# Optimization experiments

Measured on AMD Instinct MI355X. Metric: run time of the kernel, lower is better.

The kernel has to match this reference:

```python
import jax, jax.numpy as jnp
import numpy as np

EMBED_DIM = 256
NUM_HEADS = 4
LN_EPS = 1e-5


def setup_inputs() -> dict:
    b, n, e = 2, 4096, EMBED_DIM
    key = jax.random.key(0)
    ks = jax.random.split(key, 12)
    x = jax.random.normal(ks[0], (b, n, e), dtype=jnp.float32)
    # rotary cache: cos/sin of random angles, shape [2, b, n, e, 1]
    ang = jax.random.uniform(ks[1], (b, n, e, 1), dtype=jnp.float32) * (2 * np.pi)
    encoding = jnp.stack([jnp.cos(ang), jnp.sin(ang)], axis=0)
    s_e = 1.0 / np.sqrt(e)
    s_2e = 1.0 / np.sqrt(2 * e)
    Wqkv_w = jax.random.normal(ks[2], (3 * e, e), dtype=jnp.float32) * s_e
    Wqkv_b = jax.random.normal(ks[3], (3 * e,), dtype=jnp.float32) * s_e
    out_w = jax.random.normal(ks[4], (e, e), dtype=jnp.float32) * s_e
    out_b = jax.random.normal(ks[5], (e,), dtype=jnp.float32) * s_e
    ffn1_w = jax.random.normal(ks[6], (2 * e, 2 * e), dtype=jnp.float32) * s_2e
    ffn1_b = jax.random.normal(ks[7], (2 * e,), dtype=jnp.float32) * s_2e
    ln_g = jnp.ones((2 * e,), dtype=jnp.float32)
    ln_b = jnp.zeros((2 * e,), dtype=jnp.float32)
    ffn2_w = jax.random.normal(ks[8], (e, 2 * e), dtype=jnp.float32) * s_2e
    ffn2_b = jax.random.normal(ks[9], (e,), dtype=jnp.float32) * s_2e
    return {"x": x, "encoding": encoding, "Wqkv_w": Wqkv_w, "Wqkv_b": Wqkv_b,
            "out_w": out_w, "out_b": out_b, "ffn1_w": ffn1_w, "ffn1_b": ffn1_b,
            "ln_g": ln_g, "ln_b": ln_b, "ffn2_w": ffn2_w, "ffn2_b": ffn2_b}


def _forward(x, encoding, Wqkv_w, Wqkv_b, out_w, out_b, ffn1_w, ffn1_b, ln_g, ln_b, ffn2_w, ffn2_b):
    b, n, e = x.shape
    h = NUM_HEADS
    hd = e // h
    qkv = x @ Wqkv_w.T + Wqkv_b                      # [b,n,3e]
    qkv = qkv.reshape(b, n, e, 3)
    qk, v = qkv[..., :2], qkv[..., 2]                # [b,n,e,2], [b,n,e]
    # rotate_half: interpret e as (h, hd//2, 2) pairs, rotate within pairs
    r = qk.reshape(b, n, h, hd // 2, 2, 2)
    r = jnp.stack([-r[..., 1, :], r[..., 0, :]], axis=4).reshape(b, n, e, 2)
    qk = qk * encoding[0] + r * encoding[1]          # cached rotary emb
    q = qk[..., 0].reshape(b, n, h, hd)
    k = qk[..., 1].reshape(b, n, h, hd)
    vh = v.reshape(b, n, h, hd)
    scale = 1.0 / np.sqrt(hd).astype(np.float32)
    scores = jnp.einsum('bqhd,bkhd->bhqk', q, k) * scale
    attn = jax.nn.softmax(scores, axis=-1)
    ctx = jnp.einsum('bhqk,bkhd->bqhd', attn, vh).reshape(b, n, e)
    message = ctx @ out_w.T + out_b
    y = jnp.concatenate([x, message], axis=2)        # [b,n,2e]
    y = y @ ffn1_w.T + ffn1_b
    mu = jnp.mean(y, axis=-1, keepdims=True)
    var = jnp.mean(jnp.square(y - mu), axis=-1, keepdims=True)
    y = (y - mu) * jax.lax.rsqrt(var + LN_EPS) * ln_g + ln_b
    y = jax.nn.gelu(y, approximate=False)            # torch nn.GELU default = exact
    y = y @ ffn2_w.T + ffn2_b
    return x + y


def reference(x, encoding, Wqkv_w, Wqkv_b, out_w, out_b, ffn1_w, ffn1_b, ln_g, ln_b, ffn2_w, ffn2_b):
    return _forward(x, encoding, Wqkv_w, Wqkv_b, out_w, out_b, ffn1_w, ffn1_b, ln_g, ln_b, ffn2_w, ffn2_b)
```

## Files before the change

### kernel.cpp

```cpp
#include <hip/hip_runtime.h>
#include <hip/hip_bf16.h>

using u16 = unsigned short;
using u16x8 = __attribute__((ext_vector_type(8))) unsigned short;
using s16x4 = __attribute__((ext_vector_type(4))) short;
using s16x8 = __attribute__((ext_vector_type(8))) short;
using f32x4 = __attribute__((ext_vector_type(4))) float;

__device__ __forceinline__ f32x4 mfma16(s16x8 a, s16x8 b, f32x4 c) {
    return __builtin_amdgcn_mfma_f32_16x16x32_bf16(a, b, c, 0, 0, 0);
}

__device__ __forceinline__ u16 f2bf(float f) {
    union { float f; unsigned u; } v; v.f = f;
    unsigned r = v.u + 0x7FFFu + ((v.u >> 16) & 1u);
    return (u16)(r >> 16);
}

__device__ __forceinline__ unsigned cvt_pk_bf16(float lo, float hi) {
    unsigned r;
    asm("v_cvt_pk_bf16_f32 %0, %1, %2" : "=v"(r) : "v"(lo), "v"(hi));
    return r;
}

__device__ __forceinline__ float fast_exp2(float x) {
    float r;
    asm("v_exp_f32 %0, %1" : "=v"(r) : "v"(x));
    return r;
}

__device__ __forceinline__ unsigned pk2(u16 a, u16 b) {
    return (unsigned)a | ((unsigned)b << 16);
}

__device__ __forceinline__ float bf2f(u16 u) {
    union { unsigned u; float f; } v; v.u = ((unsigned)u) << 16;
    return v.f;
}

__device__ __forceinline__ void gload_lds16(const u16* g, u16* l) {
    __builtin_amdgcn_global_load_lds(
        (const __attribute__((address_space(1))) void*)g,
        (__attribute__((address_space(3))) void*)l, 16, 0, 0);
}

__global__ __launch_bounds__(256) void conv_kernel(
    const float* __restrict__ s0, const float* __restrict__ s1,
    const float* __restrict__ s2, const float* __restrict__ s3,
    const float* __restrict__ s4,
    u16* __restrict__ d0, u16* __restrict__ d1, u16* __restrict__ d2,
    u16* __restrict__ d3, u16* __restrict__ d4)
{
    int i = blockIdx.x * 256 + threadIdx.x;
    const float* s; u16* d; int off;
    if (i < 524288)      { s = s0; d = d0; off = i; }
    else if (i < 573440) { s = s1; d = d1; off = i - 524288; }
    else if (i < 589824) { s = s2; d = d2; off = i - 573440; }
    else if (i < 655360) { s = s3; d = d3; off = i - 589824; }
    else                 { s = s4; d = d4; off = i - 655360; }
    float4 f = ((const float4*)s)[off];
    ushort4 u;
    u.x = f2bf(f.x); u.y = f2bf(f.y); u.z = f2bf(f.z); u.w = f2bf(f.w);
    ((ushort4*)d)[off] = u;
}

template<int OUTMODE, bool SPLIT, bool RESID, bool BIAS, int BM>
__global__ __launch_bounds__(256) void gemm_kernel(
    const u16* __restrict__ A0, const u16* __restrict__ A1,
    const u16* __restrict__ W0, const float* __restrict__ bias,
    const float* __restrict__ resid, float* __restrict__ outf,
    u16* __restrict__ outb,
    int M, int N, int K, int lda0, int lda1, int ldw0, int ldo)
{
    constexpr int MS = BM / 32;
    __shared__ u16 A_lds[3][BM][64];
    __shared__ u16 B_lds[3][64][64];
    const int tid = threadIdx.x;
    const int l = tid & 63, w = tid >> 6;
    const int lr = l & 15, lg = l >> 4;
    const int r7 = lr & 7;
    const int m0 = blockIdx.x * BM, n0 = blockIdx.y * 64;
    const int wm = (w >> 1) * (BM / 2), wn = (w & 1) * 32;

    const int lrow = l >> 3;
    const int swz = (l & 7) ^ lrow;
    const int arow = (BM / 4) * w + lrow;
    const int brow = 16 * w + lrow;

    #define STAGE_G(s, b)                                                     \
        do {                                                                  \
            int k0_ = 64 * (s);                                               \
            const u16* As_; int lda_; int ka_ = k0_;                          \
            if (SPLIT && k0_ >= 256) { As_ = A1; lda_ = lda1; ka_ = k0_ - 256; }\
            else { As_ = A0; lda_ = lda0; }                                   \
            _Pragma("unroll")                                                 \
            for (int i = 0; i < BM / 32; ++i)                                 \
                gload_lds16(As_ + (size_t)(m0 + arow + 8 * i) * lda_ + ka_ + swz * 8,\
                            &A_lds[b][(BM / 4) * w + 8 * i][0]);              \
            _Pragma("unroll")                                                 \
            for (int i = 0; i < 2; ++i)                                       \
                gload_lds16(W0 + (size_t)(n0 + brow + 8 * i) * ldw0 + k0_ + swz * 8,\
                            &B_lds[b][16 * w + 8 * i][0]);                    \
        } while (0)

    f32x4 acc[MS][2];
    #pragma unroll
    for (int i = 0; i < MS; ++i)
        #pragma unroll
        for (int j = 0; j < 2; ++j)
            acc[i][j] = (f32x4){0.f, 0.f, 0.f, 0.f};

    const int NS = K >> 6;
    int cur = 0, nxt = 1;
    STAGE_G(0, 0);

    for (int s = 0; s < NS; ++s) {
        if (s + 1 < NS) {
            STAGE_G(s + 1, nxt);
            if constexpr (BM == 128)
                asm volatile("s_waitcnt vmcnt(6)" ::: "memory");
            else
                asm volatile("s_waitcnt vmcnt(4)" ::: "memory");
        } else {
            asm volatile("s_waitcnt vmcnt(0)" ::: "memory");
        }
        __builtin_amdgcn_sched_barrier(0);
        __builtin_amdgcn_s_barrier();
        __builtin_amdgcn_sched_barrier(0);

        #pragma unroll
        for (int ks = 0; ks < 2; ++ks) {
            s16x8 af[MS], bfr[2];
            #pragma unroll
            for (int ms = 0; ms < MS; ++ms)
                af[ms] = *(const s16x8*)&A_lds[cur][wm + ms * 16 + lr]
                                              [((ks * 4 + lg) ^ r7) * 8];
            #pragma unroll
            for (int ns = 0; ns < 2; ++ns)
                bfr[ns] = *(const s16x8*)&B_lds[cur][wn + ns * 16 + lr]
                                               [((ks * 4 + lg) ^ r7) * 8];
            #pragma unroll
            for (int ms = 0; ms < MS; ++ms)
                #pragma unroll
                for (int ns = 0; ns < 2; ++ns)
                    acc[ms][ns] = mfma16(af[ms], bfr[ns], acc[ms][ns]);
        }
        cur = nxt;
        nxt = (nxt == 2) ? 0 : nxt + 1;
    }
    #undef STAGE_G

    #pragma unroll
    for (int ms = 0; ms < MS; ++ms) {
        #pragma unroll
        for (int ns = 0; ns < 2; ++ns) {
            int cg = n0 + wn + ns * 16 + lr;
            float bv = BIAS ? bias[cg] : 0.f;
            #pragma unroll
            for (int r = 0; r < 4; ++r) {
                int rg = m0 + wm + ms * 16 + lg * 4 + r;
                float val = acc[ms][ns][r] + bv;
                if (RESID) val += resid[(size_t)rg * N + cg];
                if (OUTMODE == 0) outf[(size_t)rg * ldo + cg] = val;
                else              outb[(size_t)rg * ldo + cg] = f2bf(val);
            }
        }
    }
}

__global__ __launch_bounds__(256) void rope_tv_kernel(
    const u16* __restrict__ qkv, const float* __restrict__ enc,
    u16* __restrict__ Qo, u16* __restrict__ Ko, u16* __restrict__ Vt)
{
    __shared__ u16 vt_lds[64][72];
    const int tid = threadIdx.x;
    const int bh = blockIdx.y, n0 = blockIdx.x * 64;
    const int b = bh >> 2, h = bh & 3;
    const float qs = 0.18033688011112042f;

    #pragma unroll
    for (int it = 0; it < 8; ++it) {
        int task = it * 256 + tid;
        int r = task >> 5, t = task & 31;
        size_t grow = (size_t)(b * 4096 + n0 + r);
        const u16* base = qkv + grow * 768 + 3 * (h * 64) + 6 * t;
        ushort2 a01 = *(const ushort2*)(base);
        ushort2 a23 = *(const ushort2*)(base + 2);
        ushort2 a45 = *(const ushort2*)(base + 4);
        float q0 = bf2f(a01.x), k0 = bf2f(a01.y);
        float q1 = bf2f(a23.y), k1 = bf2f(a45.x);
        const float* cb = enc + grow * 256 + h * 64 + 2 * t;
        float2 cosv = *(const float2*)cb;
        float2 sinv = *(const float2*)(cb + 2097152);
        float qr0 = (q0 * cosv.x - q1 * sinv.x) * qs;
        float qr1 = (q1 * cosv.y + q0 * sinv.y) * qs;
        float kr0 = k0 * cosv.x - k1 * sinv.x;
        float kr1 = k1 * cosv.y + k0 * sinv.y;
        size_t o = ((size_t)bh * 4096 + n0 + r) * 64 + 2 * t;
        *(unsigned*)(Qo + o) = cvt_pk_bf16(qr0, qr1);
        *(unsigned*)(Ko + o) = cvt_pk_bf16(kr0, kr1);
        vt_lds[r][2 * t]     = a23.x;
        vt_lds[r][2 * t + 1] = a45.y;
    }
    __syncthreads();
    #pragma unroll
    for (int i = 0; i < 2; ++i) {
        int c = tid + 256 * i;
        int d = c >> 3, ng = c & 7;
        int kb = ng >> 2, lg4 = ng & 3;
        int base = 32 * kb + 4 * lg4;
        unsigned w0 = pk2(vt_lds[base +  0][d], vt_lds[base +  1][d]);
        unsigned w1 = pk2(vt_lds[base +  2][d], vt_lds[base +  3][d]);
        unsigned w2 = pk2(vt_lds[base + 16][d], vt_lds[base + 17][d]);
        unsigned w3 = pk2(vt_lds[base + 18][d], vt_lds[base + 19][d]);
        uint4 o4 = make_uint4(w0, w1, w2, w3);
        *(uint4*)(Vt + ((size_t)bh * 64 + d) * 4096 + n0 + ng * 8) = o4;
    }
}

__global__ __launch_bounds__(256) void attn_kernel(
    const u16* __restrict__ Qp, const u16* __restrict__ Kp,
    const u16* __restrict__ Vtp, u16* __restrict__ Opart,
    float* __restrict__ Ssum)
{
    __shared__ u16 K_lds[2][64][64];
    __shared__ u16 V_lds[2][64][64];
    const int tid = threadIdx.x;
    const int l = tid & 63, w = tid >> 6;
    const int lr = l & 15, lg = l >> 4;
    const int r7 = lr & 7;
    const int bh = blockIdx.y, z = blockIdx.z;
    const int n0 = blockIdx.x * 128 + w * 32;

    const u16* Qb = Qp + ((size_t)bh * 4096 + n0) * 64;
    s16x8 qf[2][2];
    #pragma unroll
    for (int qt = 0; qt < 2; ++qt)
        #pragma unroll
        for (int dh = 0; dh < 2; ++dh)
            qf[qt][dh] = *(const s16x8*)(Qb + (qt * 16 + lr) * 64 + dh * 32 + lg * 8);

    const u16* Kb = Kp + (size_t)bh * 4096 * 64 + (size_t)z * 1024 * 64;
    const u16* Vb = Vtp + (size_t)bh * 64 * 4096 + z * 1024;

    const int xs0 = (lg ^ r7) * 8;
    const int xs1 = ((4 + lg) ^ r7) * 8;

    const int swz = (l & 7) ^ ((l >> 3) & 7);
    const int row0 = 16 * w + (l >> 3);
    const size_t koff0 = (size_t)row0 * 64 + swz * 8;
    const size_t koff1 = (size_t)(row0 + 8) * 64 + swz * 8;
    const size_t voff0 = (size_t)row0 * 4096 + swz * 8;
    const size_t voff1 = (size_t)(row0 + 8) * 4096 + swz * 8;

    #define STAGE(kt, b)                                                      \
        do {                                                                  \
            const u16* ks_ = Kb + (size_t)(kt) * 4096;                        \
            const u16* vs_ = Vb + (size_t)(kt) * 64;                          \
            gload_lds16(ks_ + koff0, &K_lds[b][16 * w][0]);                   \
            gload_lds16(ks_ + koff1, &K_lds[b][16 * w + 8][0]);               \
            gload_lds16(vs_ + voff0, &V_lds[b][16 * w][0]);                   \
            gload_lds16(vs_ + voff1, &V_lds[b][16 * w + 8][0]);               \
        } while (0)

    f32x4 O[2][4];
    #pragma unroll
    for (int qt = 0; qt < 2; ++qt)
        #pragma unroll
        for (int dv = 0; dv < 4; ++dv)
            O[qt][dv] = (f32x4){0.f, 0.f, 0.f, 0.f};
    f32x4 ssum[2];
    ssum[0] = (f32x4){0.f, 0.f, 0.f, 0.f};
    ssum[1] = (f32x4){0.f, 0.f, 0.f, 0.f};
    s16x8 ones;
    #pragma unroll
    for (int j = 0; j < 8; ++j) ones[j] = (short)0x3F80;

    STAGE(0, 0);
    __syncthreads();

    #define PHASE(kt, CB, DO_STAGE)                                           \
        do {                                                                  \
            if (DO_STAGE) STAGE((kt) + 1, (CB) ^ 1);                          \
            f32x4 S[2][4];                                                    \
            __builtin_amdgcn_s_setprio(1);                                    \
            _Pragma("unroll")                                                 \
            for (int v4 = 0; v4 < 4; ++v4) {                                  \
                const int krow = v4 * 16 + lr;                                \
                s16x8 kf0 = *(const s16x8*)&K_lds[CB][krow][xs0];             \
                s16x8 kf1 = *(const s16x8*)&K_lds[CB][krow][xs1];             \
                _Pragma("unroll")                                             \
                for (int qt = 0; qt < 2; ++qt) {                              \
                    f32x4 zz = (f32x4){-24.f, -24.f, -24.f, -24.f};           \
                    zz = mfma16(kf0, qf[qt][0], zz);                          \
                    zz = mfma16(kf1, qf[qt][1], zz);                          \
                    S[qt][v4] = zz;                                           \
                }                                                             \
            }                                                                 \
            __builtin_amdgcn_s_setprio(0);                                    \
            s16x8 pa[2][2];                                                   \
            _Pragma("unroll")                                                 \
            for (int qt = 0; qt < 2; ++qt) {                                  \
                float p[4][4];                                                \
                _Pragma("unroll")                                             \
                for (int v4 = 0; v4 < 4; ++v4)                                \
                    _Pragma("unroll")                                         \
                    for (int r = 0; r < 4; ++r)                               \
                        p[v4][r] = fast_exp2(S[qt][v4][r]);                   \
                _Pragma("unroll")                                             \
                for (int kb = 0; kb < 2; ++kb) {                              \
                    union { unsigned u[4]; s16x8 v; } pu;                     \
                    pu.u[0] = cvt_pk_bf16(p[2*kb][0],   p[2*kb][1]);          \
                    pu.u[1] = cvt_pk_bf16(p[2*kb][2],   p[2*kb][3]);          \
                    pu.u[2] = cvt_pk_bf16(p[2*kb+1][0], p[2*kb+1][1]);        \
                    pu.u[3] = cvt_pk_bf16(p[2*kb+1][2], p[2*kb+1][3]);        \
                    pa[qt][kb] = pu.v;                                        \
                }                                                             \
            }                                                                 \
            __builtin_amdgcn_s_setprio(1);                                    \
            _Pragma("unroll")                                                 \
            for (int dv = 0; dv < 4; ++dv) {                                  \
                const int vrow = 16 * dv + lr;                                \
                s16x8 vf0 = *(const s16x8*)&V_lds[CB][vrow][xs0];             \
                s16x8 vf1 = *(const s16x8*)&V_lds[CB][vrow][xs1];             \
                _Pragma("unroll")                                             \
                for (int qt = 0; qt < 2; ++qt) {                              \
                    O[qt][dv] = mfma16(pa[qt][0], vf0, O[qt][dv]);            \
                    O[qt][dv] = mfma16(pa[qt][1], vf1, O[qt][dv]);            \
                }                                                             \
            }                                                                 \
            _Pragma("unroll")                                                 \
            for (int qt = 0; qt < 2; ++qt) {                                  \
                ssum[qt] = mfma16(pa[qt][0], ones, ssum[qt]);                 \
                ssum[qt] = mfma16(pa[qt][1], ones, ssum[qt]);                 \
            }                                                                 \
            __builtin_amdgcn_s_setprio(0);                                    \
            __syncthreads();                                                  \
        } while (0)

    #pragma unroll 1
    for (int kt = 0; kt < 16; kt += 2) {
        PHASE(kt, 0, true);
        PHASE(kt + 1, 1, kt < 14);
    }
    #undef PHASE
    #undef STAGE

    u16* Ob = Opart + ((size_t)(z * 8 + bh) * 4096 + n0) * 64;
    #pragma unroll
    for (int qt = 0; qt < 2; ++qt)
        #pragma unroll
        for (int dv = 0; dv < 4; ++dv)
            #pragma unroll
            for (int r = 0; r < 4; ++r)
                Ob[(size_t)(qt * 16 + 4 * lg + r) * 64 + 16 * dv + lr] =
                    f2bf(O[qt][dv][r]);
    if (lr == 0) {
        #pragma unroll
        for (int qt = 0; qt < 2; ++qt) {
            float4 sv = make_float4(ssum[qt][0], ssum[qt][1],
                                    ssum[qt][2], ssum[qt][3]);
            *(float4*)&Ssum[(size_t)(z * 8 + bh) * 4096 + n0 + qt * 16 + 4 * lg] = sv;
        }
    }
}

__global__ __launch_bounds__(256) void combine_kernel(
    const u16* __restrict__ Opart, const float* __restrict__ Ssum,
    u16* __restrict__ ctx)
{
    int idx = blockIdx.x * 256 + threadIdx.x;
    int rr = idx >> 3;
    int dc = (idx & 7) * 8;
    float s = Ssum[rr] + Ssum[32768 + rr] + Ssum[65536 + rr] + Ssum[98304 + rr];
    float inv = 1.f / s;
    float acc[8];
    #pragma unroll
    for (int j = 0; j < 8; ++j) acc[j] = 0.f;
    #pragma unroll
    for (int z = 0; z < 4; ++z) {
        u16x8 ov = *(const u16x8*)(Opart + ((size_t)z * 32768 + rr) * 64 + dc);
        #pragma unroll
        for (int j = 0; j < 8; ++j) acc[j] += bf2f(ov[j]);
    }
    #pragma unroll
    for (int j = 0; j < 8; ++j) acc[j] *= inv;
    int bh = rr >> 12, n = rr & 4095;
    int b = bh >> 2, h = bh & 3;
    uint4 o4 = make_uint4(cvt_pk_bf16(acc[0], acc[1]), cvt_pk_bf16(acc[2], acc[3]),
                          cvt_pk_bf16(acc[4], acc[5]), cvt_pk_bf16(acc[6], acc[7]));
    *(uint4*)(ctx + ((size_t)(b * 4096 + n)) * 256 + h * 64 + dc) = o4;
}

__global__ __launch_bounds__(256) void ln_gelu_kernel(
    const u16* __restrict__ y, const float* __restrict__ g,
    const float* __restrict__ bta, u16* __restrict__ o)
{
    int row = blockIdx.x * 4 + (threadIdx.x >> 6);
    int l = threadIdx.x & 63;
    const u16* yr = y + (size_t)row * 512 + l * 8;
    u16x8 uv = *(const u16x8*)yr;
    float v[8];
    #pragma unroll
    for (int j = 0; j < 8; ++j) v[j] = bf2f(uv[j]);
    float s = 0.f;
    #pragma unroll
    for (int j = 0; j < 8; ++j) s += v[j];
    #pragma unroll
    for (int off = 32; off; off >>= 1) s += __shfl_xor(s, off, 64);
    float mu = s * (1.f / 512.f);
    float q = 0.f;
    #pragma unroll
    for (int j = 0; j < 8; ++j) { float t = v[j] - mu; q += t * t; }
    #pragma unroll
    for (int off = 32; off; off >>= 1) q += __shfl_xor(q, off, 64);
    float rs = rsqrtf(q * (1.f / 512.f) + 1e-5f);
    u16 u[8];
    #pragma unroll
    for (int j = 0; j < 8; ++j) {
        float t = (v[j] - mu) * rs * g[l * 8 + j] + bta[l * 8 + j];
        t = t * 0.5f * (1.f + erff(t * 0.70710678118654752f));
        u[j] = f2bf(t);
    }
    uint4 o4 = make_uint4(pk2(u[0], u[1]), pk2(u[2], u[3]),
                          pk2(u[4], u[5]), pk2(u[6], u[7]));
    *(uint4*)(o + (size_t)row * 512 + l * 8) = o4;
}

extern "C" void kernel_launch(void* const* d_in, const int* in_sizes, int n_in,
                              void* d_out, int out_size, void* d_ws, size_t ws_size,
                              hipStream_t stream) {
    (void)in_sizes; (void)n_in; (void)out_size; (void)ws_size;
    const float* x    = (const float*)d_in[0];
    const float* enc  = (const float*)d_in[1];
    const float* wqkv = (const float*)d_in[2];
    const float* bqkv = (const float*)d_in[3];
    const float* wout = (const float*)d_in[4];
    const float* bout = (const float*)d_in[5];
    const float* w1   = (const float*)d_in[6];
    const float* b1   = (const float*)d_in[7];
    const float* lng  = (const float*)d_in[8];
    const float* lnb  = (const float*)d_in[9];
    const float* w2   = (const float*)d_in[10];
    const float* b2   = (const float*)d_in[11];
    float* out = (float*)d_out;
    char* ws = (char*)d_ws;

    u16*   xb    = (u16*)(ws + 0);
    u16*   wqkvb = (u16*)(ws + 4194304);
    u16*   woutb = (u16*)(ws + 4587520);
    u16*   w1b   = (u16*)(ws + 4718592);
    u16*   w2b   = (u16*)(ws + 5242880);
    u16*   qkvb  = (u16*)(ws + 5505024);
    u16*   OpartB= (u16*)(ws + 5505024);
    u16*   y1bf  = (u16*)(ws + 5505024);
    float* Ssum  = (float*)(ws + 22282240);
    u16*   q     = (u16*)(ws + 30670848);
    u16*   k     = (u16*)(ws + 34865152);
    u16*   vt    = (u16*)(ws + 43253760);
    u16*   ybf   = q;
    u16*   ctx   = (u16*)(ws + 47448064);
    u16*   msg   = (u16*)(ws + 51642368);

    conv_kernel<<<2688, 256, 0, stream>>>(x, wqkv, wout, w1, w2,
                                          xb, wqkvb, woutb, w1b, w2b);
    gemm_kernel<1, false, false, true, 128><<<dim3(64, 12), 256, 0, stream>>>(
        xb, nullptr, wqkvb, bqkv, nullptr, nullptr, qkvb,
        8192, 768, 256, 256, 0, 256, 768);
    rope_tv_kernel<<<dim3(64, 8), 256, 0, stream>>>(qkvb, enc, q, k, vt);
    attn_kernel<<<dim3(32, 8, 4), 256, 0, stream>>>(q, k, vt, OpartB, Ssum);
    combine_kernel<<<1024, 256, 0, stream>>>(OpartB, Ssum, ctx);
    gemm_kernel<1, false, false, true, 64><<<dim3(128, 4), 256, 0, stream>>>(
        ctx, nullptr, woutb, bout, nullptr, nullptr, msg,
        8192, 256, 256, 256, 0, 256, 256);
    gemm_kernel<1, true, false, true, 128><<<dim3(64, 8), 256, 0, stream>>>(
        xb, msg, w1b, b1, nullptr, nullptr, y1bf,
        8192, 512, 512, 256, 256, 512, 512);
    ln_gelu_kernel<<<2048, 256, 0, stream>>>(y1bf, lng, lnb, ybf);
    gemm_kernel<0, false, true, true, 64><<<dim3(128, 4), 256, 0, stream>>>(
        ybf, nullptr, w2b, b2, x, out, nullptr,
        8192, 256, 512, 512, 0, 512, 256);
}
```

Baseline: 116.5 us.

## Double per-wave query rows in attention and split key block into two passes

```diff
diff --git a/kernel.cpp b/kernel.cpp
--- a/kernel.cpp
+++ b/kernel.cpp
@@ -230,12 +230,12 @@
     const int lr = l & 15, lg = l >> 4;
     const int r7 = lr & 7;
     const int bh = blockIdx.y, z = blockIdx.z;
-    const int n0 = blockIdx.x * 128 + w * 32;
+    const int n0 = blockIdx.x * 256 + w * 64;
 
     const u16* Qb = Qp + ((size_t)bh * 4096 + n0) * 64;
-    s16x8 qf[2][2];
-    #pragma unroll
-    for (int qt = 0; qt < 2; ++qt)
+    s16x8 qf[4][2];
+    #pragma unroll
+    for (int qt = 0; qt < 4; ++qt)
         #pragma unroll
         for (int dh = 0; dh < 2; ++dh)
             qf[qt][dh] = *(const s16x8*)(Qb + (qt * 16 + lr) * 64 + dh * 32 + lg * 8);
@@ -263,78 +263,80 @@
             gload_lds16(vs_ + voff1, &V_lds[b][16 * w + 8][0]);               \
         } while (0)
 
-    f32x4 O[2][4];
-    #pragma unroll
-    for (int qt = 0; qt < 2; ++qt)
+    f32x4 O[4][4];
+    #pragma unroll
+    for (int qt = 0; qt < 4; ++qt)
         #pragma unroll
         for (int dv = 0; dv < 4; ++dv)
             O[qt][dv] = (f32x4){0.f, 0.f, 0.f, 0.f};
-    f32x4 ssum[2];
-    ssum[0] = (f32x4){0.f, 0.f, 0.f, 0.f};
-    ssum[1] = (f32x4){0.f, 0.f, 0.f, 0.f};
+    f32x4 ssum[4];
+    #pragma unroll
+    for (int qt = 0; qt < 4; ++qt) ssum[qt] = (f32x4){0.f, 0.f, 0.f, 0.f};
     s16x8 ones;
     #pragma unroll
     for (int j = 0; j < 8; ++j) ones[j] = (short)0x3F80;
 
     STAGE(0, 0);
     __syncthreads();
+
+    #define KBPASS(CB, KB)                                                    \
+        do {                                                                  \
+            const int rA = (2 * (KB)) * 16 + lr;                              \
+            const int rB = (2 * (KB) + 1) * 16 + lr;                          \
+            s16x8 kfA0 = *(const s16x8*)&K_lds[CB][rA][xs0];                  \
+            s16x8 kfA1 = *(const s16x8*)&K_lds[CB][rA][xs1];                  \
+            s16x8 kfB0 = *(const s16x8*)&K_lds[CB][rB][xs0];                  \
+            s16x8 kfB1 = *(const s16x8*)&K_lds[CB][rB][xs1];                  \
+            f32x4 SA[4], SB[4];                                               \
+            __builtin_amdgcn_s_setprio(1);                                    \
+            _Pragma("unroll")                                                 \
+            for (int qt = 0; qt < 4; ++qt) {                                  \
+                f32x4 za = (f32x4){-24.f, -24.f, -24.f, -24.f};               \
+                za = mfma16(kfA0, qf[qt][0], za);                             \
+                za = mfma16(kfA1, qf[qt][1], za);                             \
+                SA[qt] = za;                                                  \
+                f32x4 zb = (f32x4){-24.f, -24.f, -24.f, -24.f};               \
+                zb = mfma16(kfB0, qf[qt][0], zb);                             \
+                zb = mfma16(kfB1, qf[qt][1], zb);                             \
+                SB[qt] = zb;                                                  \
+            }                                                                 \
+            __builtin_amdgcn_s_setprio(0);                                    \
+            s16x8 pa[4];                                                      \
+            _Pragma("unroll")                                                 \
+            for (int qt = 0; qt < 4; ++qt) {                                  \
+                union { unsigned u[4]; s16x8 v; } pu;                         \
+                pu.u[0] = cvt_pk_bf16(fast_exp2(SA[qt][0]),                   \
+                                      fast_exp2(SA[qt][1]));                  \
+                pu.u[1] = cvt_pk_bf16(fast_exp2(SA[qt][2]),                   \
+                                      fast_exp2(SA[qt][3]));                  \
+                pu.u[2] = cvt_pk_bf16(fast_exp2(SB[qt][0]),                   \
+                                      fast_exp2(SB[qt][1]));                  \
+                pu.u[3] = cvt_pk_bf16(fast_exp2(SB[qt][2]),                   \
+                                      fast_exp2(SB[qt][3]));                  \
+                pa[qt] = pu.v;                                                \
+            }                                                                 \
+            const int vs_ = (KB) ? xs1 : xs0;                                 \
+            s16x8 vf0 = *(const s16x8*)&V_lds[CB][lr][vs_];                   \
+            s16x8 vf1 = *(const s16x8*)&V_lds[CB][16 + lr][vs_];              \
+            s16x8 vf2 = *(const s16x8*)&V_lds[CB][32 + lr][vs_];              \
+            s16x8 vf3 = *(const s16x8*)&V_lds[CB][48 + lr][vs_];              \
+            __builtin_amdgcn_s_setprio(1);                                    \
+            _Pragma("unroll")                                                 \
+            for (int qt = 0; qt < 4; ++qt) {                                  \
+                O[qt][0] = mfma16(pa[qt], vf0, O[qt][0]);                     \
+                O[qt][1] = mfma16(pa[qt], vf1, O[qt][1]);                     \
+                O[qt][2] = mfma16(pa[qt], vf2, O[qt][2]);                     \
+                O[qt][3] = mfma16(pa[qt], vf3, O[qt][3]);                     \
+                ssum[qt] = mfma16(pa[qt], ones, ssum[qt]);                    \
+            }                                                                 \
+            __builtin_amdgcn_s_setprio(0);                                    \
+        } while (0)
 
     #define PHASE(kt, CB, DO_STAGE)                                           \
         do {                                                                  \
             if (DO_STAGE) STAGE((kt) + 1, (CB) ^ 1);                          \
-            f32x4 S[2][4];                                                    \
-            __builtin_amdgcn_s_setprio(1);                                    \
-            _Pragma("unroll")                                                 \
-            for (int v4 = 0; v4 < 4; ++v4) {                                  \
-                const int krow = v4 * 16 + lr;                                \
-                s16x8 kf0 = *(const s16x8*)&K_lds[CB][krow][xs0];             \
-                s16x8 kf1 = *(const s16x8*)&K_lds[CB][krow][xs1];             \
-                _Pragma("unroll")                                             \
-                for (int qt = 0; qt < 2; ++qt) {                              \
-                    f32x4 zz = (f32x4){-24.f, -24.f, -24.f, -24.f};           \
-                    zz = mfma16(kf0, qf[qt][0], zz);                          \
-                    zz = mfma16(kf1, qf[qt][1], zz);                          \
-                    S[qt][v4] = zz;                                           \
-                }                                                             \
-            }                                                                 \
-            __builtin_amdgcn_s_setprio(0);                                    \
-            s16x8 pa[2][2];                                                   \
-            _Pragma("unroll")                                                 \
-            for (int qt = 0; qt < 2; ++qt) {                                  \
-                float p[4][4];                                                \
-                _Pragma("unroll")                                             \
-                for (int v4 = 0; v4 < 4; ++v4)                                \
-                    _Pragma("unroll")                                         \
-                    for (int r = 0; r < 4; ++r)                               \
-                        p[v4][r] = fast_exp2(S[qt][v4][r]);                   \
-                _Pragma("unroll")                                             \
-                for (int kb = 0; kb < 2; ++kb) {                              \
-                    union { unsigned u[4]; s16x8 v; } pu;                     \
-                    pu.u[0] = cvt_pk_bf16(p[2*kb][0],   p[2*kb][1]);          \
-                    pu.u[1] = cvt_pk_bf16(p[2*kb][2],   p[2*kb][3]);          \
-                    pu.u[2] = cvt_pk_bf16(p[2*kb+1][0], p[2*kb+1][1]);        \
-                    pu.u[3] = cvt_pk_bf16(p[2*kb+1][2], p[2*kb+1][3]);        \
-                    pa[qt][kb] = pu.v;                                        \
-                }                                                             \
-            }                                                                 \
-            __builtin_amdgcn_s_setprio(1);                                    \
-            _Pragma("unroll")                                                 \
-            for (int dv = 0; dv < 4; ++dv) {                                  \
-                const int vrow = 16 * dv + lr;                                \
-                s16x8 vf0 = *(const s16x8*)&V_lds[CB][vrow][xs0];             \
-                s16x8 vf1 = *(const s16x8*)&V_lds[CB][vrow][xs1];             \
-                _Pragma("unroll")                                             \
-                for (int qt = 0; qt < 2; ++qt) {                              \
-                    O[qt][dv] = mfma16(pa[qt][0], vf0, O[qt][dv]);            \
-                    O[qt][dv] = mfma16(pa[qt][1], vf1, O[qt][dv]);            \
-                }                                                             \
-            }                                                                 \
-            _Pragma("unroll")                                                 \
-            for (int qt = 0; qt < 2; ++qt) {                                  \
-                ssum[qt] = mfma16(pa[qt][0], ones, ssum[qt]);                 \
-                ssum[qt] = mfma16(pa[qt][1], ones, ssum[qt]);                 \
-            }                                                                 \
-            __builtin_amdgcn_s_setprio(0);                                    \
+            KBPASS(CB, 0);                                                    \
+            KBPASS(CB, 1);                                                    \
             __syncthreads();                                                  \
         } while (0)
 
@@ -344,11 +346,12 @@
         PHASE(kt + 1, 1, kt < 14);
     }
     #undef PHASE
+    #undef KBPASS
     #undef STAGE
 
     u16* Ob = Opart + ((size_t)(z * 8 + bh) * 4096 + n0) * 64;
     #pragma unroll
-    for (int qt = 0; qt < 2; ++qt)
+    for (int qt = 0; qt < 4; ++qt)
         #pragma unroll
         for (int dv = 0; dv < 4; ++dv)
             #pragma unroll
@@ -357,7 +360,7 @@
                     f2bf(O[qt][dv][r]);
     if (lr == 0) {
         #pragma unroll
-        for (int qt = 0; qt < 2; ++qt) {
+        for (int qt = 0; qt < 4; ++qt) {
             float4 sv = make_float4(ssum[qt][0], ssum[qt][1],
                                     ssum[qt][2], ssum[qt][3]);
             *(float4*)&Ssum[(size_t)(z * 8 + bh) * 4096 + n0 + qt * 16 + 4 * lg] = sv;
@@ -468,7 +471,7 @@
         xb, nullptr, wqkvb, bqkv, nullptr, nullptr, qkvb,
         8192, 768, 256, 256, 0, 256, 768);
     rope_tv_kernel<<<dim3(64, 8), 256, 0, stream>>>(qkvb, enc, q, k, vt);
-    attn_kernel<<<dim3(32, 8, 4), 256, 0, stream>>>(q, k, vt, OpartB, Ssum);
+    attn_kernel<<<dim3(16, 8, 4), 256, 0, stream>>>(q, k, vt, OpartB, Ssum);
     combine_kernel<<<1024, 256, 0, stream>>>(OpartB, Ssum, ctx);
     gemm_kernel<1, false, false, true, 64><<<dim3(128, 4), 256, 0, stream>>>(
         ctx, nullptr, woutb, bout, nullptr, nullptr, msg,
```

After: 124.6 us. 6.9% more time.

## Fuse split-K attention combine into the output projection GEMM

Applied to the files above, without the earlier changes.

```diff
diff --git a/kernel.cpp b/kernel.cpp
--- a/kernel.cpp
+++ b/kernel.cpp
@@ -365,31 +365,117 @@
     }
 }
 
-__global__ __launch_bounds__(256) void combine_kernel(
+__global__ __launch_bounds__(256) void ctxproj_kernel(
     const u16* __restrict__ Opart, const float* __restrict__ Ssum,
-    u16* __restrict__ ctx)
+    const u16* __restrict__ W0, const float* __restrict__ bias,
+    u16* __restrict__ msg)
 {
-    int idx = blockIdx.x * 256 + threadIdx.x;
-    int rr = idx >> 3;
-    int dc = (idx & 7) * 8;
-    float s = Ssum[rr] + Ssum[32768 + rr] + Ssum[65536 + rr] + Ssum[98304 + rr];
-    float inv = 1.f / s;
-    float acc[8];
-    #pragma unroll
-    for (int j = 0; j < 8; ++j) acc[j] = 0.f;
-    #pragma unroll
-    for (int z = 0; z < 4; ++z) {
-        u16x8 ov = *(const u16x8*)(Opart + ((size_t)z * 32768 + rr) * 64 + dc);
-        #pragma unroll
-        for (int j = 0; j < 8; ++j) acc[j] += bf2f(ov[j]);
-    }
-    #pragma unroll
-    for (int j = 0; j < 8; ++j) acc[j] *= inv;
-    int bh = rr >> 12, n = rr & 4095;
-    int b = bh >> 2, h = bh & 3;
-    uint4 o4 = make_uint4(cvt_pk_bf16(acc[0], acc[1]), cvt_pk_bf16(acc[2], acc[3]),
-                          cvt_pk_bf16(acc[4], acc[5]), cvt_pk_bf16(acc[6], acc[7]));
-    *(uint4*)(ctx + ((size_t)(b * 4096 + n)) * 256 + h * 64 + dc) = o4;
+    __shared__ u16 A_lds[64][264];
+    __shared__ u16 B_lds[3][64][64];
+    const int tid = threadIdx.x;
+    const int l = tid & 63, w = tid >> 6;
+    const int lr = l & 15, lg = l >> 4;
+    const int r7 = lr & 7;
+    const int m0 = blockIdx.x * 64, n0 = blockIdx.y * 64;
+    const int wm = (w >> 1) * 32, wn = (w & 1) * 32;
+
+    const int lrow = l >> 3;
+    const int swz = (l & 7) ^ lrow;
+    const int brow = 16 * w + lrow;
+
+    #define STAGE_B(s, bb)                                                    \
+        do {                                                                  \
+            _Pragma("unroll")                                                 \
+            for (int i = 0; i < 2; ++i)                                       \
+                gload_lds16(W0 + (size_t)(n0 + brow + 8 * i) * 256 + 64 * (s) \
+                                + swz * 8,                                    \
+                            &B_lds[bb][16 * w + 8 * i][0]);                   \
+        } while (0)
+
+    STAGE_B(0, 0);
+
+    {
+        const int row = tid >> 2, h = tid & 3;
+        const int rr = m0 + row;
+        const int b = rr >> 12, n = rr & 4095;
+        const size_t sb = (size_t)(b * 4 + h) * 4096 + n;
+        float s = Ssum[sb] + Ssum[32768 + sb] + Ssum[65536 + sb] + Ssum[98304 + sb];
+        float inv = 1.f / s;
+        const size_t ob = sb * 64;
+        #pragma unroll 2
+        for (int j = 0; j < 8; ++j) {
+            float acc[8];
+            #pragma unroll
+            for (int e = 0; e < 8; ++e) acc[e] = 0.f;
+            #pragma unroll
+            for (int z = 0; z < 4; ++z) {
+                u16x8 ov = *(const u16x8*)(Opart + (size_t)z * 2097152 + ob + j * 8);
+                #pragma unroll
+                for (int e = 0; e < 8; ++e) acc[e] += bf2f(ov[e]);
+            }
+            uint4 o4 = make_uint4(cvt_pk_bf16(acc[0] * inv, acc[1] * inv),
+                                  cvt_pk_bf16(acc[2] * inv, acc[3] * inv),
+                                  cvt_pk_bf16(acc[4] * inv, acc[5] * inv),
+                                  cvt_pk_bf16(acc[6] * inv, acc[7] * inv));
+            *(uint4*)&A_lds[row][h * 64 + j * 8] = o4;
+        }
+    }
+    __syncthreads();
+
+    f32x4 acc[2][2];
+    #pragma unroll
+    for (int i = 0; i < 2; ++i)
+        #pragma unroll
+        for (int j = 0; j < 2; ++j)
+            acc[i][j] = (f32x4){0.f, 0.f, 0.f, 0.f};
+
+    int cur = 0, nxt = 1;
+    for (int s = 0; s < 4; ++s) {
+        if (s + 1 < 4) {
+            STAGE_B(s + 1, nxt);
+            asm volatile("s_waitcnt vmcnt(2)" ::: "memory");
+        } else {
+            asm volatile("s_waitcnt vmcnt(0)" ::: "memory");
+        }
+        __builtin_amdgcn_sched_barrier(0);
+        __builtin_amdgcn_s_barrier();
+        __builtin_amdgcn_sched_barrier(0);
+
+        #pragma unroll
+        for (int ks = 0; ks < 2; ++ks) {
+            s16x8 af[2], bfr[2];
+            #pragma unroll
+            for (int ms = 0; ms < 2; ++ms)
+                af[ms] = *(const s16x8*)&A_lds[wm + ms * 16 + lr]
+                                              [64 * s + (ks * 4 + lg) * 8];
+            #pragma unroll
+            for (int ns = 0; ns < 2; ++ns)
+                bfr[ns] = *(const s16x8*)&B_lds[cur][wn + ns * 16 + lr]
+                                               [((ks * 4 + lg) ^ r7) * 8];
+            #pragma unroll
+            for (int ms = 0; ms < 2; ++ms)
+                #pragma unroll
+                for (int ns = 0; ns < 2; ++ns)
+                    acc[ms][ns] = mfma16(af[ms], bfr[ns], acc[ms][ns]);
+        }
+        cur = nxt;
+        nxt = (nxt == 2) ? 0 : nxt + 1;
+    }
+    #undef STAGE_B
+
+    #pragma unroll
+    for (int ms = 0; ms < 2; ++ms) {
+        #pragma unroll
+        for (int ns = 0; ns < 2; ++ns) {
+            int cg = n0 + wn + ns * 16 + lr;
+            float bv = bias[cg];
+            #pragma unroll
+            for (int r = 0; r < 4; ++r) {
+                int rg = m0 + wm + ms * 16 + lg * 4 + r;
+                msg[(size_t)rg * 256 + cg] = f2bf(acc[ms][ns][r] + bv);
+            }
+        }
+    }
 }
 
 __global__ __launch_bounds__(256) void ln_gelu_kernel(
@@ -459,7 +545,6 @@
     u16*   k     = (u16*)(ws + 34865152);
     u16*   vt    = (u16*)(ws + 43253760);
     u16*   ybf   = q;
-    u16*   ctx   = (u16*)(ws + 47448064);
     u16*   msg   = (u16*)(ws + 51642368);
 
     conv_kernel<<<2688, 256, 0, stream>>>(x, wqkv, wout, w1, w2,
@@ -469,10 +554,7 @@
         8192, 768, 256, 256, 0, 256, 768);
     rope_tv_kernel<<<dim3(64, 8), 256, 0, stream>>>(qkvb, enc, q, k, vt);
     attn_kernel<<<dim3(32, 8, 4), 256, 0, stream>>>(q, k, vt, OpartB, Ssum);
-    combine_kernel<<<1024, 256, 0, stream>>>(OpartB, Ssum, ctx);
-    gemm_kernel<1, false, false, true, 64><<<dim3(128, 4), 256, 0, stream>>>(
-        ctx, nullptr, woutb, bout, nullptr, nullptr, msg,
-        8192, 256, 256, 256, 0, 256, 256);
+    ctxproj_kernel<<<dim3(128, 4), 256, 0, stream>>>(OpartB, Ssum, woutb, bout, msg);
     gemm_kernel<1, true, false, true, 128><<<dim3(64, 8), 256, 0, stream>>>(
         xb, msg, w1b, b1, nullptr, nullptr, y1bf,
         8192, 512, 512, 256, 256, 512, 512);
```

Measured after the change: 122.9 us. 1.05x slower.
